# Kernel tuning notes

Measured on AMD Instinct MI355X. Metric: run time of the kernel, lower is better.

The kernel has to match this reference:

```python
import jax, jax.numpy as jnp
import numpy as np

TIME_DIM = 2
DIM = 512
N_ENT = 100000
N_REL = 500
B = 512
K = 128
MARGIN = 2.0
EPS = 1e-6


def proj_tan0(u):
    # tangent space at origin o=(1,0,...,0): first coordinate zeroed
    return u.at[..., 0].set(0.0)


def expmap0(u):
    # exponential map at the origin of the pseudo-hyperboloid Q^{s,t}, beta=-1.
    # quadratic norm of tangent vector (time dims negative): branch on sign.
    u = proj_tan0(u)
    a = -jnp.sum(u[..., :TIME_DIM] ** 2, axis=-1) + jnp.sum(u[..., TIME_DIM:] ** 2, axis=-1)
    sp = jnp.sqrt(jnp.clip(a, EPS))   # space-like branch radius
    st = jnp.sqrt(jnp.clip(-a, EPS))  # time-like branch radius
    c = jnp.where(a > 0, jnp.cosh(sp), jnp.cos(st))
    s = jnp.where(a > 0, jnp.sinh(sp) / sp, jnp.sin(st) / st)
    o = jnp.zeros_like(u).at[..., 0].set(1.0)
    return c[..., None] * o + s[..., None] * u


def _norm_givens(r):
    g = r.reshape(r.shape[0], -1, 2)
    return g / jnp.clip(jnp.linalg.norm(g, axis=-1, keepdims=True), 1e-15)


def givens_rotations(r, x):
    g = _norm_givens(r)
    xp = x.reshape(r.shape[0], -1, 2)
    c, s = g[..., 0:1], g[..., 1:2]
    x0, x1 = xp[..., 0:1], xp[..., 1:2]
    out = jnp.concatenate([c * x0 - s * x1, c * x1 + s * x0], axis=-1)
    return out.reshape(r.shape[0], -1)


def givens_reflection(r, x):
    g = _norm_givens(r)
    xp = x.reshape(r.shape[0], -1, 2)
    c, s = g[..., 0:1], g[..., 1:2]
    x0, x1 = xp[..., 0:1], xp[..., 1:2]
    out = jnp.concatenate([c * x0 + s * x1, s * x0 - c * x1], axis=-1)
    return out.reshape(r.shape[0], -1)


def manhattan_sqdist(x, y):
    # Manhattan-style geodesic on Q^{s,t} via the S^{t-1} x H^s decomposition:
    # leg 1: rotate time direction on the sphere of radius ||x_t||,
    # leg 2: hyperbolic distance along the shared time direction. Asymmetric
    # in (x, y), hence the min over both orders in the caller.
    xt, xs = x[..., :TIME_DIM], x[..., TIME_DIM:]
    yt, ys = y[..., :TIME_DIM], y[..., TIME_DIM:]
    nx = jnp.linalg.norm(xt, axis=-1)
    ny = jnp.linalg.norm(yt, axis=-1)
    cosang = jnp.clip(jnp.sum(xt * yt, axis=-1) / (nx * ny), -1.0 + EPS, 1.0 - EPS)
    d_sph = nx * jnp.arccos(cosang)
    inner = nx * ny - jnp.sum(xs * ys, axis=-1)
    d_hyp = jnp.arccosh(jnp.clip(inner, 1.0 + EPS))
    return (d_sph + d_hyp) ** 2


def setup_inputs() -> dict:
    key = jax.random.key(0)
    ks = jax.random.split(key, 8)
    emb_entity = jax.random.normal(ks[0], (N_ENT, DIM), jnp.float32)
    relation_boost = 1e-5 * jax.nn.softplus(jax.random.normal(ks[1], (N_REL, TIME_DIM), jnp.float32))
    relation_rot_left = 2.0 * jax.random.uniform(ks[2], (N_REL, DIM), jnp.float32) - 1.0
    relation_rot_right = 2.0 * jax.random.uniform(ks[3], (N_REL, DIM), jnp.float32) - 1.0
    bias_head = jnp.zeros((N_ENT,), jnp.float32)
    bias_tail = jnp.zeros((N_ENT,), jnp.float32)
    u_idx = jax.random.randint(ks[4], (B,), 0, N_ENT)
    r_idx = jax.random.randint(ks[5], (B,), 0, N_REL)
    v_idx = jax.random.randint(ks[6], (B, K), 0, N_ENT)
    return {"emb_entity": emb_entity, "relation_boost": relation_boost,
            "relation_rot_left": relation_rot_left, "relation_rot_right": relation_rot_right,
            "bias_head": bias_head, "bias_tail": bias_tail,
            "u_idx": u_idx, "r_idx": r_idx, "v_idx": v_idx}


def reference(emb_entity, relation_boost, relation_rot_left, relation_rot_right,
              bias_head, bias_tail, u_idx, r_idx, v_idx):
    head = emb_entity[u_idx]                       # [B, D]
    tail = emb_entity[v_idx]                       # [B, K, D]
    b = jax.nn.softplus(relation_boost[r_idx])     # [B, 2]
    r_left = relation_rot_left[r_idx]
    r_right = relation_rot_right[r_idx]

    head = expmap0(head)
    tail = expmap0(proj_tan0(tail))

    head = givens_rotations(r_right, head)

    # dense (D x D) Lorentz boost per example, faithful to the original matmul
    C = jnp.sqrt(1.0 + b ** 2)
    t_idx = jnp.arange(TIME_DIM)
    bt_idx = DIM - TIME_DIM + jnp.arange(TIME_DIM)
    m_idx = jnp.arange(TIME_DIM, DIM - TIME_DIM)
    boost = jnp.zeros((b.shape[0], DIM, DIM), head.dtype)
    boost = boost.at[:, t_idx, t_idx].set(C)
    boost = boost.at[:, bt_idx, bt_idx].set(C)
    boost = boost.at[:, t_idx, bt_idx].set(-b)
    boost = boost.at[:, bt_idx, t_idx].set(-b)
    boost = boost.at[:, m_idx, m_idx].set(1.0)
    head = jnp.einsum('bij,bj->bi', boost, head)

    head = givens_reflection(r_left, head)

    # pairwise manifold distance, min over the two Manhattan-path orders
    c1 = manhattan_sqdist(head[:, None, :], tail)  # [B, K]
    c2 = manhattan_sqdist(tail, head[:, None, :])
    dist = jnp.minimum(c1, c2)

    return MARGIN - dist + bias_head[u_idx][:, None] + bias_tail[v_idx]
```

## Files before the change

kernel.cpp:

```cpp
#include <hip/hip_runtime.h>
#include <math.h>

#define DIM_ 512
#define K_ 128
#define EPS_ 1e-6f
#define MARGIN_ 2.0f

__device__ __forceinline__ float wsum(float v) {
#pragma unroll
    for (int off = 32; off >= 1; off >>= 1)
        v += __shfl_xor(v, off, 64);
    return v;
}

__device__ __forceinline__ void givens_rot(float gc, float gs, float& x0, float& x1) {
    float n = fmaxf(sqrtf(gc * gc + gs * gs), 1e-15f);
    float c = gc / n, s = gs / n;
    float y0 = c * x0 - s * x1;
    float y1 = c * x1 + s * x0;
    x0 = y0; x1 = y1;
}

__device__ __forceinline__ void givens_ref(float gc, float gs, float& x0, float& x1) {
    float n = fmaxf(sqrtf(gc * gc + gs * gs), 1e-15f);
    float c = gc / n, s = gs / n;
    float y0 = c * x0 + s * x1;
    float y1 = s * x0 - c * x1;
    x0 = y0; x1 = y1;
}

__global__ __launch_bounds__(256) void ultrae_kernel(
    const float* __restrict__ emb,
    const float* __restrict__ rel_boost,
    const float* __restrict__ rot_left,
    const float* __restrict__ rot_right,
    const float* __restrict__ bias_head,
    const float* __restrict__ bias_tail,
    const int* __restrict__ u_idx,
    const int* __restrict__ r_idx,
    const int* __restrict__ v_idx,
    float* __restrict__ out)
{
    const int b = blockIdx.x;
    const int lane = threadIdx.x & 63;
    const int wave = threadIdx.x >> 6;
    const int u = u_idx[b];
    const int r = r_idx[b];

    const float* hrow = emb + (size_t)u * DIM_ + lane * 8;
    float4 h0 = *(const float4*)hrow;
    float4 h1 = *(const float4*)(hrow + 4);
    if (lane == 0) h0.x = 0.f;
    float ps = h0.x*h0.x + h0.y*h0.y + h0.z*h0.z + h0.w*h0.w
             + h1.x*h1.x + h1.y*h1.y + h1.z*h1.z + h1.w*h1.w;
    float tot = wsum(ps);
    float u1 = __shfl(h0.y, 0, 64);
    float a = tot - 2.f * u1 * u1;
    float ch, sh;
    if (a > 0.f) {
        float sp = sqrtf(fmaxf(a, EPS_));
        ch = coshf(sp); sh = sinhf(sp) / sp;
    } else {
        float st = sqrtf(fmaxf(-a, EPS_));
        ch = cosf(st); sh = sinf(st) / st;
    }
    h0.x *= sh; h0.y *= sh; h0.z *= sh; h0.w *= sh;
    h1.x *= sh; h1.y *= sh; h1.z *= sh; h1.w *= sh;
    if (lane == 0) h0.x = ch;

    const float* rr = rot_right + (size_t)r * DIM_ + lane * 8;
    float4 g0 = *(const float4*)rr;
    float4 g1 = *(const float4*)(rr + 4);
    givens_rot(g0.x, g0.y, h0.x, h0.y);
    givens_rot(g0.z, g0.w, h0.z, h0.w);
    givens_rot(g1.x, g1.y, h1.x, h1.y);
    givens_rot(g1.z, g1.w, h1.z, h1.w);

    float bb0 = log1pf(expf(rel_boost[2*r]));
    float bb1 = log1pf(expf(rel_boost[2*r+1]));
    float C0 = sqrtf(1.f + bb0*bb0);
    float C1 = sqrtf(1.f + bb1*bb1);
    float e0   = __shfl(h0.x, 0, 64);
    float e1   = __shfl(h0.y, 0, 64);
    float e510 = __shfl(h1.z, 63, 64);
    float e511 = __shfl(h1.w, 63, 64);
    if (lane == 0) {
        h0.x = C0*e0 - bb0*e510;
        h0.y = C1*e1 - bb1*e511;
    }
    if (lane == 63) {
        h1.z = C0*e510 - bb0*e0;
        h1.w = C1*e511 - bb1*e1;
    }

    const float* rl = rot_left + (size_t)r * DIM_ + lane * 8;
    g0 = *(const float4*)rl;
    g1 = *(const float4*)(rl + 4);
    givens_ref(g0.x, g0.y, h0.x, h0.y);
    givens_ref(g0.z, g0.w, h0.z, h0.w);
    givens_ref(g1.x, g1.y, h1.x, h1.y);
    givens_ref(g1.z, g1.w, h1.z, h1.w);

    float hf0 = __shfl(h0.x, 0, 64);
    float hf1 = __shfl(h0.y, 0, 64);
    float nx = sqrtf(hf0*hf0 + hf1*hf1);
    if (lane == 0) { h0.x = 0.f; h0.y = 0.f; }
    float bh = bias_head[u];

    const int kbase = (blockIdx.y * 4 + wave) * 8;
    const int* vp = v_idx + b * K_ + kbase;

#pragma unroll
    for (int i = 0; i < 8; ++i) {
        int v = vp[i];
        const float* trow = emb + (size_t)v * DIM_ + lane * 8;
        float4 t0 = *(const float4*)trow;
        float4 t1 = *(const float4*)(trow + 4);
        float tt1 = __shfl(t0.y, 0, 64);
        if (lane == 0) { t0.x = 0.f; t0.y = 0.f; }
        float q = t0.x*t0.x + t0.y*t0.y + t0.z*t0.z + t0.w*t0.w
                + t1.x*t1.x + t1.y*t1.y + t1.z*t1.z + t1.w*t1.w;
        float d = h0.x*t0.x + h0.y*t0.y + h0.z*t0.z + h0.w*t0.w
                + h1.x*t1.x + h1.y*t1.y + h1.z*t1.z + h1.w*t1.w;
#pragma unroll
        for (int off = 32; off >= 1; off >>= 1) {
            q += __shfl_xor(q, off, 64);
            d += __shfl_xor(d, off, 64);
        }
        float at = q - tt1 * tt1;
        float ct, st;
        if (at > 0.f) {
            float sp = sqrtf(fmaxf(at, EPS_));
            ct = coshf(sp); st = sinhf(sp) / sp;
        } else {
            float s2 = sqrtf(fmaxf(-at, EPS_));
            ct = cosf(s2); st = sinf(s2) / s2;
        }
        float yt1 = st * tt1;
        float ny = sqrtf(ct*ct + yt1*yt1);
        float dott = hf0*ct + hf1*yt1;
        float cosang = dott / (nx * ny);
        cosang = fminf(fmaxf(cosang, -1.f + EPS_), 1.f - EPS_);
        float ang = acosf(cosang);
        float dsph = fminf(nx, ny) * ang;
        float inner = fmaxf(nx*ny - st*d, 1.f + EPS_);
        float dhyp = acoshf(inner);
        float dsum = dsph + dhyp;
        if (lane == 0) {
            out[b * K_ + kbase + i] = MARGIN_ - dsum*dsum + bh + bias_tail[v];
        }
    }
}

extern "C" void kernel_launch(void* const* d_in, const int* in_sizes, int n_in,
                              void* d_out, int out_size, void* d_ws, size_t ws_size,
                              hipStream_t stream) {
    const float* emb       = (const float*)d_in[0];
    const float* rel_boost = (const float*)d_in[1];
    const float* rot_left  = (const float*)d_in[2];
    const float* rot_right = (const float*)d_in[3];
    const float* bias_h    = (const float*)d_in[4];
    const float* bias_t    = (const float*)d_in[5];
    const int* u_idx       = (const int*)d_in[6];
    const int* r_idx       = (const int*)d_in[7];
    const int* v_idx       = (const int*)d_in[8];
    float* out = (float*)d_out;

    int B = in_sizes[6];
    dim3 grid(B, 4), block(256);
    hipLaunchKernelGGL(ultrae_kernel, grid, block, 0, stream,
                       emb, rel_boost, rot_left, rot_right,
                       bias_h, bias_t, u_idx, r_idx, v_idx, out);
}
```

Baseline: 286.2 us.

## Prefetch tail rows up front, double grid split, and use fast transcendentals

```diff
diff --git a/kernel.cpp b/kernel.cpp
--- a/kernel.cpp
+++ b/kernel.cpp
@@ -5,25 +5,51 @@
 #define K_ 128
 #define EPS_ 1e-6f
 #define MARGIN_ 2.0f
+#define PI_ 3.14159265358979f
 
-__device__ __forceinline__ float wsum(float v) {
-#pragma unroll
-    for (int off = 32; off >= 1; off >>= 1)
-        v += __shfl_xor(v, off, 64);
-    return v;
+__device__ __forceinline__ float frcp(float x) { return __builtin_amdgcn_rcpf(x); }
+
+__device__ __forceinline__ float fast_acos(float x) {
+    float ax = fabsf(x);
+    float p = -0.0187293f;
+    p = p * ax + 0.0742610f;
+    p = p * ax - 0.2121144f;
+    p = p * ax + 1.5707288f;
+    float r = sqrtf(fmaxf(1.f - ax, 0.f)) * p;
+    return x < 0.f ? PI_ - r : r;
+}
+
+__device__ __forceinline__ void fast_coshsinh(float x, float& c, float& s) {
+    float e  = __expf(x);
+    float ei = frcp(e);
+    c = 0.5f * (e + ei);
+    s = 0.5f * (e - ei);
+}
+
+__device__ __forceinline__ void expmap_cs(float a, float& c, float& s) {
+    if (a > 0.f) {
+        float sp = sqrtf(fmaxf(a, EPS_));
+        float ch, sh;
+        fast_coshsinh(sp, ch, sh);
+        c = ch; s = sh * frcp(sp);
+    } else {
+        float st = sqrtf(fmaxf(-a, EPS_));
+        c = __cosf(st);
+        s = __sinf(st) * frcp(st);
+    }
 }
 
 __device__ __forceinline__ void givens_rot(float gc, float gs, float& x0, float& x1) {
-    float n = fmaxf(sqrtf(gc * gc + gs * gs), 1e-15f);
-    float c = gc / n, s = gs / n;
+    float rn = frcp(fmaxf(sqrtf(gc * gc + gs * gs), 1e-15f));
+    float c = gc * rn, s = gs * rn;
     float y0 = c * x0 - s * x1;
     float y1 = c * x1 + s * x0;
     x0 = y0; x1 = y1;
 }
 
 __device__ __forceinline__ void givens_ref(float gc, float gs, float& x0, float& x1) {
-    float n = fmaxf(sqrtf(gc * gc + gs * gs), 1e-15f);
-    float c = gc / n, s = gs / n;
+    float rn = frcp(fmaxf(sqrtf(gc * gc + gs * gs), 1e-15f));
+    float c = gc * rn, s = gs * rn;
     float y0 = c * x0 + s * x1;
     float y1 = s * x0 - c * x1;
     x0 = y0; x1 = y1;
@@ -47,81 +73,88 @@
     const int u = u_idx[b];
     const int r = r_idx[b];
 
+    const int kbase = (blockIdx.y * 4 + wave) * 4;
+    const int4 vv = *(const int4*)(v_idx + b * K_ + kbase);
+    const int vi[4] = {vv.x, vv.y, vv.z, vv.w};
+    float4 t0[4], t1[4];
+#pragma unroll
+    for (int i = 0; i < 4; ++i) {
+        const float* trow = emb + (size_t)vi[i] * DIM_ + lane * 8;
+        t0[i] = *(const float4*)trow;
+        t1[i] = *(const float4*)(trow + 4);
+    }
+
     const float* hrow = emb + (size_t)u * DIM_ + lane * 8;
     float4 h0 = *(const float4*)hrow;
     float4 h1 = *(const float4*)(hrow + 4);
     if (lane == 0) h0.x = 0.f;
     float ps = h0.x*h0.x + h0.y*h0.y + h0.z*h0.z + h0.w*h0.w
              + h1.x*h1.x + h1.y*h1.y + h1.z*h1.z + h1.w*h1.w;
-    float tot = wsum(ps);
+#pragma unroll
+    for (int off = 32; off >= 1; off >>= 1) ps += __shfl_xor(ps, off, 64);
     float u1 = __shfl(h0.y, 0, 64);
-    float a = tot - 2.f * u1 * u1;
+    float a = ps - 2.f * u1 * u1;
     float ch, sh;
-    if (a > 0.f) {
-        float sp = sqrtf(fmaxf(a, EPS_));
-        ch = coshf(sp); sh = sinhf(sp) / sp;
-    } else {
-        float st = sqrtf(fmaxf(-a, EPS_));
-        ch = cosf(st); sh = sinf(st) / st;
-    }
+    expmap_cs(a, ch, sh);
     h0.x *= sh; h0.y *= sh; h0.z *= sh; h0.w *= sh;
     h1.x *= sh; h1.y *= sh; h1.z *= sh; h1.w *= sh;
     if (lane == 0) h0.x = ch;
 
-    const float* rr = rot_right + (size_t)r * DIM_ + lane * 8;
-    float4 g0 = *(const float4*)rr;
-    float4 g1 = *(const float4*)(rr + 4);
-    givens_rot(g0.x, g0.y, h0.x, h0.y);
-    givens_rot(g0.z, g0.w, h0.z, h0.w);
-    givens_rot(g1.x, g1.y, h1.x, h1.y);
-    givens_rot(g1.z, g1.w, h1.z, h1.w);
-
-    float bb0 = log1pf(expf(rel_boost[2*r]));
-    float bb1 = log1pf(expf(rel_boost[2*r+1]));
-    float C0 = sqrtf(1.f + bb0*bb0);
-    float C1 = sqrtf(1.f + bb1*bb1);
-    float e0   = __shfl(h0.x, 0, 64);
-    float e1   = __shfl(h0.y, 0, 64);
-    float e510 = __shfl(h1.z, 63, 64);
-    float e511 = __shfl(h1.w, 63, 64);
-    if (lane == 0) {
-        h0.x = C0*e0 - bb0*e510;
-        h0.y = C1*e1 - bb1*e511;
-    }
-    if (lane == 63) {
-        h1.z = C0*e510 - bb0*e0;
-        h1.w = C1*e511 - bb1*e1;
+    {
+        const float* rr = rot_right + (size_t)r * DIM_ + lane * 8;
+        float4 g0 = *(const float4*)rr;
+        float4 g1 = *(const float4*)(rr + 4);
+        givens_rot(g0.x, g0.y, h0.x, h0.y);
+        givens_rot(g0.z, g0.w, h0.z, h0.w);
+        givens_rot(g1.x, g1.y, h1.x, h1.y);
+        givens_rot(g1.z, g1.w, h1.z, h1.w);
     }
 
-    const float* rl = rot_left + (size_t)r * DIM_ + lane * 8;
-    g0 = *(const float4*)rl;
-    g1 = *(const float4*)(rl + 4);
-    givens_ref(g0.x, g0.y, h0.x, h0.y);
-    givens_ref(g0.z, g0.w, h0.z, h0.w);
-    givens_ref(g1.x, g1.y, h1.x, h1.y);
-    givens_ref(g1.z, g1.w, h1.z, h1.w);
+    {
+        float bb0 = __logf(1.f + __expf(rel_boost[2*r]));
+        float bb1 = __logf(1.f + __expf(rel_boost[2*r+1]));
+        float C0 = sqrtf(1.f + bb0*bb0);
+        float C1 = sqrtf(1.f + bb1*bb1);
+        float e0   = __shfl(h0.x, 0, 64);
+        float e1   = __shfl(h0.y, 0, 64);
+        float e510 = __shfl(h1.z, 63, 64);
+        float e511 = __shfl(h1.w, 63, 64);
+        if (lane == 0) {
+            h0.x = C0*e0 - bb0*e510;
+            h0.y = C1*e1 - bb1*e511;
+        }
+        if (lane == 63) {
+            h1.z = C0*e510 - bb0*e0;
+            h1.w = C1*e511 - bb1*e1;
+        }
+    }
+
+    {
+        const float* rl = rot_left + (size_t)r * DIM_ + lane * 8;
+        float4 g0 = *(const float4*)rl;
+        float4 g1 = *(const float4*)(rl + 4);
+        givens_ref(g0.x, g0.y, h0.x, h0.y);
+        givens_ref(g0.z, g0.w, h0.z, h0.w);
+        givens_ref(g1.x, g1.y, h1.x, h1.y);
+        givens_ref(g1.z, g1.w, h1.z, h1.w);
+    }
 
     float hf0 = __shfl(h0.x, 0, 64);
     float hf1 = __shfl(h0.y, 0, 64);
     float nx = sqrtf(hf0*hf0 + hf1*hf1);
     if (lane == 0) { h0.x = 0.f; h0.y = 0.f; }
-    float bh = bias_head[u];
-
-    const int kbase = (blockIdx.y * 4 + wave) * 8;
-    const int* vp = v_idx + b * K_ + kbase;
+    const float bh = bias_head[u];
+    const float rnx = frcp(nx);
 
 #pragma unroll
-    for (int i = 0; i < 8; ++i) {
-        int v = vp[i];
-        const float* trow = emb + (size_t)v * DIM_ + lane * 8;
-        float4 t0 = *(const float4*)trow;
-        float4 t1 = *(const float4*)(trow + 4);
-        float tt1 = __shfl(t0.y, 0, 64);
-        if (lane == 0) { t0.x = 0.f; t0.y = 0.f; }
-        float q = t0.x*t0.x + t0.y*t0.y + t0.z*t0.z + t0.w*t0.w
-                + t1.x*t1.x + t1.y*t1.y + t1.z*t1.z + t1.w*t1.w;
-        float d = h0.x*t0.x + h0.y*t0.y + h0.z*t0.z + h0.w*t0.w
-                + h1.x*t1.x + h1.y*t1.y + h1.z*t1.z + h1.w*t1.w;
+    for (int i = 0; i < 4; ++i) {
+        float4 s0 = t0[i], s1 = t1[i];
+        float tt1 = __shfl(s0.y, 0, 64);
+        if (lane == 0) { s0.x = 0.f; s0.y = 0.f; }
+        float q = s0.x*s0.x + s0.y*s0.y + s0.z*s0.z + s0.w*s0.w
+                + s1.x*s1.x + s1.y*s1.y + s1.z*s1.z + s1.w*s1.w;
+        float d = h0.x*s0.x + h0.y*s0.y + h0.z*s0.z + h0.w*s0.w
+                + h1.x*s1.x + h1.y*s1.y + h1.z*s1.z + h1.w*s1.w;
 #pragma unroll
         for (int off = 32; off >= 1; off >>= 1) {
             q += __shfl_xor(q, off, 64);
@@ -129,25 +162,17 @@
         }
         float at = q - tt1 * tt1;
         float ct, st;
-        if (at > 0.f) {
-            float sp = sqrtf(fmaxf(at, EPS_));
-            ct = coshf(sp); st = sinhf(sp) / sp;
-        } else {
-            float s2 = sqrtf(fmaxf(-at, EPS_));
-            ct = cosf(s2); st = sinf(s2) / s2;
-        }
+        expmap_cs(at, ct, st);
         float yt1 = st * tt1;
         float ny = sqrtf(ct*ct + yt1*yt1);
-        float dott = hf0*ct + hf1*yt1;
-        float cosang = dott / (nx * ny);
+        float cosang = (hf0*ct + hf1*yt1) * rnx * frcp(ny);
         cosang = fminf(fmaxf(cosang, -1.f + EPS_), 1.f - EPS_);
-        float ang = acosf(cosang);
-        float dsph = fminf(nx, ny) * ang;
+        float dsph = fminf(nx, ny) * fast_acos(cosang);
         float inner = fmaxf(nx*ny - st*d, 1.f + EPS_);
-        float dhyp = acoshf(inner);
+        float dhyp = __logf(inner + sqrtf(inner - 1.f) * sqrtf(inner + 1.f));
         float dsum = dsph + dhyp;
         if (lane == 0) {
-            out[b * K_ + kbase + i] = MARGIN_ - dsum*dsum + bh + bias_tail[v];
+            out[b * K_ + kbase + i] = MARGIN_ - dsum*dsum + bh + bias_tail[vi[i]];
         }
     }
 }
@@ -167,7 +192,7 @@
     float* out = (float*)d_out;
 
     int B = in_sizes[6];
-    dim3 grid(B, 4), block(256);
+    dim3 grid(B, 8), block(256);
     hipLaunchKernelGGL(ultrae_kernel, grid, block, 0, stream,
                        emb, rel_boost, rot_left, rot_right,
                        bias_h, bias_t, u_idx, r_idx, v_idx, out);
```

After: 279.4 us. 2.4% less time.
